# Kernel tuning notes

Hardware: AMD Instinct MI355X
Metric: run time of the kernel (lower is better)

## Reference

```python
import jax, jax.numpy as jnp
import numpy as np

BS, N, D, H = 4, 2048, 512, 8
DK = D // H
XAVIER_STD = float(np.sqrt(2.0 / (D + D)))  # xavier_normal_, gain=1


def setup_inputs() -> dict:
    key = jax.random.key(0)
    ks = jax.random.split(key, 10)
    Q = jax.random.normal(ks[0], (BS, N, D), jnp.float32)
    K = jax.random.normal(ks[1], (BS, N, D), jnp.float32)
    V = jax.random.normal(ks[2], (BS, N, D), jnp.float32)
    q_mas = jax.random.randint(ks[3], (BS, N, 1), 0, 2).astype(jnp.float32)
    k_mas = jax.random.randint(ks[4], (BS, N, 1), 0, 2).astype(jnp.float32)
    # 0/1 attention mask; force self-edges so no row is fully masked (avoids NaN softmax)
    att_mas = jax.random.randint(ks[5], (BS, N, N), 0, 2).astype(jnp.float32)
    att_mas = jnp.maximum(att_mas, jnp.eye(N, dtype=jnp.float32)[None])
    WQ = jax.random.normal(ks[6], (D, D), jnp.float32) * XAVIER_STD
    WK = jax.random.normal(ks[7], (D, D), jnp.float32) * XAVIER_STD
    WV = jax.random.normal(ks[8], (D, D), jnp.float32) * XAVIER_STD
    WO = jax.random.normal(ks[9], (D, D), jnp.float32) * XAVIER_STD
    return {"Q": Q, "K": K, "V": V, "q_mas": q_mas, "k_mas": k_mas,
            "att_mas": att_mas, "WQ": WQ, "WK": WK, "WV": WV, "WO": WO}


def reference(Q, K, V, q_mas, k_mas, att_mas, WQ, WK, WV, WO):
    bs, n, d = Q.shape
    h, dk = H, DK
    qm = q_mas.reshape(bs, 1, n, 1)  # (bs,1,n,1)
    km = k_mas.reshape(bs, 1, n, 1)
    # nn.Linear (no bias): x @ W.T ; split heads -> (bs,h,n,dk); apply pre-masks
    Qh = qm * (Q @ WQ.T).reshape(bs, n, h, dk).transpose(0, 2, 1, 3)
    Kh = km * (K @ WK.T).reshape(bs, n, h, dk).transpose(0, 2, 1, 3)
    Vh = km * (V @ WV.T).reshape(bs, n, h, dk).transpose(0, 2, 1, 3)
    scores = jnp.einsum('bhqd,bhkd->bhqk', Qh, Kh) / jnp.sqrt(jnp.float32(dk))
    mas = att_mas.reshape(bs, 1, n, n)
    scores = jnp.where(mas.astype(bool), scores, -jnp.inf)
    attn = jax.nn.softmax(scores, axis=-1) * mas
    y = jnp.einsum('bhqk,bhkd->bhqd', attn, Vh) * km  # post-mask (note: km over query dim, as in source)
    y = y.transpose(0, 2, 1, 3).reshape(bs, n, d)
    y = (y @ WO.T) * k_mas.reshape(bs, n, 1)
    return y
```

## Files before the change

### kernel.cpp

```cpp
#include <hip/hip_runtime.h>


#define BS_    4
#define NSEQ   2048
#define DMODEL 512
#define NH     8
#define DKH    64
#define MROWS  (BS_ * NSEQ)
#define NW32   (NSEQ / 32)
#define NWORDS (BS_ * NSEQ * NSEQ / 32)

typedef unsigned short ushort_t;
typedef __attribute__((ext_vector_type(8))) short short8;
typedef __attribute__((ext_vector_type(4))) float floatx4;

__device__ __forceinline__ ushort_t f2bf(float f) {
    unsigned int x = __builtin_bit_cast(unsigned int, f);
    unsigned int lsb = (x >> 16) & 1u;
    x += 0x7fffu + lsb;
    return (ushort_t)(x >> 16);
}
__device__ __forceinline__ floatx4 mfma_bf16(short8 a, short8 b, floatx4 c) {
    return __builtin_amdgcn_mfma_f32_16x16x32_bf16(a, b, c, 0, 0, 0);
}
__device__ __forceinline__ void gld16(const ushort_t* g, ushort_t* l) {
    __builtin_amdgcn_global_load_lds(
        (const __attribute__((address_space(1))) unsigned int*)g,
        (__attribute__((address_space(3))) unsigned int*)l, 16, 0, 0);
}
__device__ __forceinline__ unsigned int cvt_pk_bf16(float lo, float hi) {
    unsigned int r;
    asm("v_cvt_pk_bf16_f32 %0, %1, %2" : "=v"(r) : "v"(lo), "v"(hi));
    return r;
}
__device__ __forceinline__ float fexp2(float x) {
#if __has_builtin(__builtin_amdgcn_exp2f)
    return __builtin_amdgcn_exp2f(x);
#else
    return exp2f(x);
#endif
}
__device__ __forceinline__ void permlane32_swap(unsigned& a, unsigned& b) {
    asm volatile("v_permlane32_swap_b32 %0, %1" : "+v"(a), "+v"(b));
}
__device__ __forceinline__ void permlane16_swap(unsigned& a, unsigned& b) {
    asm volatile("v_permlane16_swap_b32 %0, %1" : "+v"(a), "+v"(b));
}

__global__ __launch_bounds__(256) void cvt_all(const float* __restrict__ a,
                                               const float* __restrict__ b,
                                               const float* __restrict__ c,
                                               const float* __restrict__ wq,
                                               const float* __restrict__ wk,
                                               const float* __restrict__ wv,
                                               const float* __restrict__ wo,
                                               const float* __restrict__ am,
                                               ushort_t* __restrict__ dst,
                                               ushort_t* __restrict__ wdst,
                                               unsigned int* __restrict__ mb, int n4) {
    const int i = blockIdx.x * blockDim.x + threadIdx.x;
    const int yy = blockIdx.y;
    if (yy == 4) {
        if (i < NWORDS) {
            const float4* src = (const float4*)am + (size_t)i * 8;
            unsigned int m = 0;
#pragma unroll
            for (int j = 0; j < 8; ++j) {
                const float4 v = src[j];
                m |= (v.x != 0.f ? 1u : 0u) << (4 * j);
                m |= (v.y != 0.f ? 1u : 0u) << (4 * j + 1);
                m |= (v.z != 0.f ? 1u : 0u) << (4 * j + 2);
                m |= (v.w != 0.f ? 1u : 0u) << (4 * j + 3);
            }
            mb[i] = m;
        }
        return;
    }
    if (yy == 3) {
        const int wn4 = DMODEL * DMODEL / 4;
        if (i < 4 * wn4) {
            const int w = i >> 16;
            const float* src = (w == 0) ? wq : (w == 1) ? wk : (w == 2) ? wv : wo;
            const float4 v = ((const float4*)src)[i & (wn4 - 1)];
            ushort4 o;
            o.x = f2bf(v.x); o.y = f2bf(v.y); o.z = f2bf(v.z); o.w = f2bf(v.w);
            ((ushort4*)wdst)[i] = o;
        }
        return;
    }
    const float* src = (yy == 0) ? a : (yy == 1) ? b : c;
    ushort_t* d = dst + (size_t)yy * ((size_t)n4 * 4);
    const float4 v = ((const float4*)src)[i];
    ushort4 o;
    o.x = f2bf(v.x); o.y = f2bf(v.y); o.z = f2bf(v.z); o.w = f2bf(v.w);
    ((ushort4*)d)[i] = o;
}

__global__ __launch_bounds__(256) void gemm_proj(const ushort_t* __restrict__ Xall,
                                                 const ushort_t* __restrict__ Wall,
                                                 const float* __restrict__ qmas,
                                                 const float* __restrict__ kmas,
                                                 ushort_t* __restrict__ Qh,
                                                 ushort_t* __restrict__ Kh,
                                                 ushort_t* __restrict__ Vt) {
    __shared__ ushort_t As[128 * 64];
    __shared__ ushort_t Bs[128 * 64];
    const int z = blockIdx.z;
    const ushort_t* X  = Xall + (size_t)z * MROWS * DMODEL;
    const ushort_t* Wb = Wall + (size_t)z * DMODEL * DMODEL;
    const float* rowmask = (z == 0) ? qmas : kmas;

    const int tid  = threadIdx.x;
    const int wave = tid >> 6;
    const int lane = tid & 63;
    const int l16  = lane & 15;
    const int quad = lane >> 4;
    const int wr   = wave >> 1;
    const int wc   = wave & 1;
    const int m0   = blockIdx.x * 128;
    const int n0   = blockIdx.y * 128;
    const int srow = tid >> 3;
    const int scol = 8 * ((tid & 7) ^ ((tid >> 3) & 7));

    floatx4 acc[4][4];
#pragma unroll
    for (int t = 0; t < 4; ++t)
#pragma unroll
        for (int u = 0; u < 4; ++u) acc[t][u] = (floatx4){0.f, 0.f, 0.f, 0.f};

    for (int k0 = 0; k0 < DMODEL; k0 += 64) {
#pragma unroll
        for (int i = 0; i < 4; ++i) {
            const int row = i * 32 + srow;
            gld16(X  + (size_t)(m0 + row) * DMODEL + k0 + scol, &As[i * 2048 + tid * 8]);
            gld16(Wb + (size_t)(n0 + row) * DMODEL + k0 + scol, &Bs[i * 2048 + tid * 8]);
        }
        __syncthreads();
#pragma unroll
        for (int kk = 0; kk < 64; kk += 32) {
            short8 a[4], b[4];
#pragma unroll
            for (int t = 0; t < 4; ++t) {
                const int pc = ((((kk >> 3) | quad) ^ (l16 & 7)) * 8);
                a[t] = *(const short8*)&As[(wr * 64 + t * 16 + l16) * 64 + pc];
            }
#pragma unroll
            for (int u = 0; u < 4; ++u) {
                const int pc = ((((kk >> 3) | quad) ^ (l16 & 7)) * 8);
                b[u] = *(const short8*)&Bs[(wc * 64 + u * 16 + l16) * 64 + pc];
            }
#pragma unroll
            for (int t = 0; t < 4; ++t)
#pragma unroll
                for (int u = 0; u < 4; ++u) acc[t][u] = mfma_bf16(a[t], b[u], acc[t][u]);
        }
        __syncthreads();
    }

    float rm[4][4];
#pragma unroll
    for (int t = 0; t < 4; ++t)
#pragma unroll
        for (int r = 0; r < 4; ++r)
            rm[t][r] = rowmask[m0 + wr * 64 + t * 16 + quad * 4 + r];
    if (z == 0) {
#pragma unroll
        for (int t = 0; t < 4; ++t)
#pragma unroll
            for (int r = 0; r < 4; ++r) rm[t][r] *= 0.18033688011112042f;
    }

    const int bb    = m0 >> 11;
    const int nbase = (m0 & (NSEQ - 1)) + wr * 64;
#pragma unroll
    for (int t = 0; t < 4; ++t) {
#pragma unroll
        for (int u = 0; u < 4; ++u) {
            const int d = n0 + wc * 64 + u * 16 + l16;
            const int h = d >> 6, cc = d & 63;
            if (z < 2) {
                ushort_t* dst = (z == 0) ? Qh : Kh;
#pragma unroll
                for (int r = 0; r < 4; ++r) {
                    const int n = nbase + t * 16 + quad * 4 + r;
                    dst[((size_t)(bb * NH + h) * NSEQ + n) * DKH + cc] =
                        f2bf(acc[t][u][r] * rm[t][r]);
                }
            } else {
                ushort4 pk;
                pk.x = f2bf(acc[t][u][0] * rm[t][0]);
                pk.y = f2bf(acc[t][u][1] * rm[t][1]);
                pk.z = f2bf(acc[t][u][2] * rm[t][2]);
                pk.w = f2bf(acc[t][u][3] * rm[t][3]);
                const int n = nbase + t * 16 + quad * 4;
                *(ushort4*)(Vt + ((size_t)(bb * NH + h) * DKH + cc) * NSEQ + n) = pk;
            }
        }
    }
}

__global__ __launch_bounds__(256) void gemm_out(const ushort_t* __restrict__ X,
                                                const ushort_t* __restrict__ Wb,
                                                const float* __restrict__ rowmask,
                                                float* __restrict__ dst) {
    __shared__ ushort_t As[128 * 64];
    __shared__ ushort_t Bs[128 * 64];
    const int tid  = threadIdx.x;
    const int wave = tid >> 6;
    const int lane = tid & 63;
    const int l16  = lane & 15;
    const int quad = lane >> 4;
    const int wr   = wave >> 1;
    const int wc   = wave & 1;
    const int m0   = blockIdx.x * 128;
    const int n0   = blockIdx.y * 128;
    const int srow = tid >> 3;
    const int scol = 8 * ((tid & 7) ^ ((tid >> 3) & 7));

    floatx4 acc[4][4];
#pragma unroll
    for (int t = 0; t < 4; ++t)
#pragma unroll
        for (int u = 0; u < 4; ++u) acc[t][u] = (floatx4){0.f, 0.f, 0.f, 0.f};

    for (int k0 = 0; k0 < DMODEL; k0 += 64) {
#pragma unroll
        for (int i = 0; i < 4; ++i) {
            const int row = i * 32 + srow;
            gld16(X  + (size_t)(m0 + row) * DMODEL + k0 + scol, &As[i * 2048 + tid * 8]);
            gld16(Wb + (size_t)(n0 + row) * DMODEL + k0 + scol, &Bs[i * 2048 + tid * 8]);
        }
        __syncthreads();
#pragma unroll
        for (int kk = 0; kk < 64; kk += 32) {
            short8 a[4], b[4];
#pragma unroll
            for (int t = 0; t < 4; ++t) {
                const int pc = ((((kk >> 3) | quad) ^ (l16 & 7)) * 8);
                a[t] = *(const short8*)&As[(wr * 64 + t * 16 + l16) * 64 + pc];
            }
#pragma unroll
            for (int u = 0; u < 4; ++u) {
                const int pc = ((((kk >> 3) | quad) ^ (l16 & 7)) * 8);
                b[u] = *(const short8*)&Bs[(wc * 64 + u * 16 + l16) * 64 + pc];
            }
#pragma unroll
            for (int t = 0; t < 4; ++t)
#pragma unroll
                for (int u = 0; u < 4; ++u) acc[t][u] = mfma_bf16(a[t], b[u], acc[t][u]);
        }
        __syncthreads();
    }

#pragma unroll
    for (int t = 0; t < 4; ++t) {
#pragma unroll
        for (int r = 0; r < 4; ++r) {
            const int m = m0 + wr * 64 + t * 16 + quad * 4 + r;
            const float rm = rowmask[m];
#pragma unroll
            for (int u = 0; u < 4; ++u) {
                const int d = n0 + wc * 64 + u * 16 + l16;
                dst[(size_t)m * DMODEL + d] = acc[t][u][r] * rm;
            }
        }
    }
}

__global__ __launch_bounds__(256) void attn_kernel(const ushort_t* __restrict__ Qh,
                                                   const ushort_t* __restrict__ Kh,
                                                   const ushort_t* __restrict__ Vt,
                                                   const unsigned int* __restrict__ Mb,
                                                   const float* __restrict__ kmas,
                                                   ushort_t* __restrict__ y) {
    __shared__ __align__(16) ushort_t Ks[128 * 72];
    __shared__ __align__(16) ushort_t Vs[64 * 136];

    const int tid  = threadIdx.x;
    const int lane = tid & 63;
    const int wave = tid >> 6;
    const int l16  = lane & 15;
    const int quad = lane >> 4;
    const int h    = blockIdx.y;
    const int b    = blockIdx.z;
    const int qw   = blockIdx.x * 128 + wave * 32;

    const ushort_t* Kb = Kh + (size_t)(b * NH + h) * NSEQ * DKH;
    const ushort_t* Vb = Vt + (size_t)(b * NH + h) * DKH * NSEQ;
    const uint4* Mv0 = (const uint4*)(Mb + ((size_t)(b * NSEQ + qw) + l16) * NW32);
    const uint4* Mv1 = (const uint4*)(Mb + ((size_t)(b * NSEQ + qw) + 16 + l16) * NW32);

    const ushort_t* Qp0 = Qh + ((size_t)((b * NH + h) * NSEQ) + qw + l16) * DKH + quad * 8;
    const ushort_t* Qp1 = Qp0 + 16 * DKH;
    const short8 qf0a = *(const short8*)Qp0;
    const short8 qf0b = *(const short8*)(Qp0 + 32);
    const short8 qf1a = *(const short8*)Qp1;
    const short8 qf1b = *(const short8*)(Qp1 + 32);

    const short8 ones = {(short)0x3F80, (short)0x3F80, (short)0x3F80, (short)0x3F80,
                         (short)0x3F80, (short)0x3F80, (short)0x3F80, (short)0x3F80};

    floatx4 accA[4], accB[4];
    floatx4 accL0 = (floatx4){0.f, 0.f, 0.f, 0.f};
    floatx4 accL1 = (floatx4){0.f, 0.f, 0.f, 0.f};
#pragma unroll
    for (int ct = 0; ct < 4; ++ct) {
        accA[ct] = (floatx4){0.f, 0.f, 0.f, 0.f};
        accB[ct] = (floatx4){0.f, 0.f, 0.f, 0.f};
    }

#define SFRAG(FR, PX0, PY0, PX1, PY1) do {                                         \
    const short8 ka = *(const short8*)&Ks[((FR) * 16 + l16) * 72 + quad * 8];      \
    const short8 kb = *(const short8*)&Ks[((FR) * 16 + l16) * 72 + 32 + quad * 8]; \
    floatx4 s0 = {0.f, 0.f, 0.f, 0.f};                                             \
    s0 = mfma_bf16(ka, qf0a, s0);                                                  \
    s0 = mfma_bf16(kb, qf0b, s0);                                                  \
    floatx4 s1 = {0.f, 0.f, 0.f, 0.f};                                             \
    s1 = mfma_bf16(ka, qf1a, s1);                                                  \
    s1 = mfma_bf16(kb, qf1b, s1);                                                  \
    float p0[4], p1[4];                                                            \
    _Pragma("unroll")                                                              \
    for (int r = 0; r < 4; ++r) {                                                  \
        const int bitp = (((FR) & 1) << 4) + r;                                    \
        const unsigned m0m =                                                       \
            (unsigned)__builtin_amdgcn_sbfe((int)wsh0[(FR) >> 1], bitp, 1);        \
        const unsigned m1m =                                                       \
            (unsigned)__builtin_amdgcn_sbfe((int)wsh1[(FR) >> 1], bitp, 1);        \
        p0[r] = __builtin_bit_cast(float,                                          \
                    __builtin_bit_cast(unsigned, fexp2(s0[r])) & m0m);             \
        p1[r] = __builtin_bit_cast(float,                                          \
                    __builtin_bit_cast(unsigned, fexp2(s1[r])) & m1m);             \
    }                                                                              \
    PX0 = cvt_pk_bf16(p0[0], p0[1]); PY0 = cvt_pk_bf16(p0[2], p0[3]);              \
    PX1 = cvt_pk_bf16(p1[0], p1[1]); PY1 = cvt_pk_bf16(p1[2], p1[3]);              \
} while (0)

    for (int kt = 0; kt < NSEQ / 128; ++kt) {
        const int k0 = kt * 128;

        short8 kv[4], vv[4];
#pragma unroll
        for (int i = 0; i < 4; ++i) {
            const int c = tid + i * 256;
            kv[i] = *(const short8*)(Kb + (size_t)(k0 + (c >> 3)) * DKH + (c & 7) * 8);
        }
#pragma unroll
        for (int i = 0; i < 4; ++i) {
            const int c = tid + i * 256;
            vv[i] = *(const short8*)(Vb + (size_t)(c >> 4) * NSEQ + k0 + (c & 15) * 8);
        }
        const uint4 mw0 = Mv0[kt];
        const uint4 mw1 = Mv1[kt];

        __syncthreads();
#pragma unroll
        for (int i = 0; i < 4; ++i) {
            const int c = tid + i * 256;
            *(short8*)&Ks[(c >> 3) * 72 + (c & 7) * 8] = kv[i];
        }
#pragma unroll
        for (int i = 0; i < 4; ++i) {
            const int c = tid + i * 256;
            *(short8*)&Vs[(c >> 4) * 136 + (c & 15) * 8] = vv[i];
        }
        __syncthreads();

        const unsigned int wsh0[4] = {mw0.x >> (quad * 4), mw0.y >> (quad * 4),
                                      mw0.z >> (quad * 4), mw0.w >> (quad * 4)};
        const unsigned int wsh1[4] = {mw1.x >> (quad * 4), mw1.y >> (quad * 4),
                                      mw1.z >> (quad * 4), mw1.w >> (quad * 4)};

#pragma unroll
        for (int kf = 0; kf < 4; ++kf) {
            unsigned xe0, ye0, xo0, yo0;
            unsigned xe1, ye1, xo1, yo1;
            SFRAG(kf * 2,     xe0, ye0, xe1, ye1);
            SFRAG(kf * 2 + 1, xo0, yo0, xo1, yo1);

            permlane32_swap(xe0, xo0); permlane32_swap(ye0, yo0);
            permlane16_swap(xe0, xo0); permlane16_swap(ye0, yo0);
            permlane32_swap(xe1, xo1); permlane32_swap(ye1, yo1);
            permlane16_swap(xe1, xo1); permlane16_swap(ye1, yo1);

            const uint4 u0 = {xe0, ye0, xo0, yo0};
            const uint4 u1 = {xe1, ye1, xo1, yo1};
            const short8 pf0 = __builtin_bit_cast(short8, u0);
            const short8 pf1 = __builtin_bit_cast(short8, u1);

            accL0 = mfma_bf16(pf0, ones, accL0);
            accL1 = mfma_bf16(pf1, ones, accL1);

#pragma unroll
            for (int ct = 0; ct < 4; ++ct) {
                const short8 vb =
                    *(const short8*)&Vs[(ct * 16 + l16) * 136 + kf * 32 + quad * 8];
                accA[ct] = mfma_bf16(pf0, vb, accA[ct]);
                accB[ct] = mfma_bf16(pf1, vb, accB[ct]);
            }
        }
    }
#undef SFRAG

#pragma unroll
    for (int r = 0; r < 4; ++r) {
        const int q0 = qw + quad * 4 + r;
        const int q1 = q0 + 16;
        const float sc0 = kmas[b * NSEQ + q0] / accL0[r];
        const float sc1 = kmas[b * NSEQ + q1] / accL1[r];
#pragma unroll
        for (int ct = 0; ct < 4; ++ct) {
            y[(size_t)(b * NSEQ + q0) * DMODEL + h * DKH + ct * 16 + l16] =
                f2bf(accA[ct][r] * sc0);
            y[(size_t)(b * NSEQ + q1) * DMODEL + h * DKH + ct * 16 + l16] =
                f2bf(accB[ct][r] * sc1);
        }
    }
}

extern "C" void kernel_launch(void* const* d_in, const int* in_sizes, int n_in,
                              void* d_out, int out_size, void* d_ws, size_t ws_size,
                              hipStream_t stream) {
    (void)in_sizes; (void)n_in; (void)out_size; (void)ws_size;
    const float* Q  = (const float*)d_in[0];
    const float* K  = (const float*)d_in[1];
    const float* V  = (const float*)d_in[2];
    const float* qm = (const float*)d_in[3];
    const float* km = (const float*)d_in[4];
    const float* am = (const float*)d_in[5];
    const float* WQ = (const float*)d_in[6];
    const float* WK = (const float*)d_in[7];
    const float* WV = (const float*)d_in[8];
    const float* WO = (const float*)d_in[9];

    const size_t XN = (size_t)MROWS * DMODEL;
    const size_t WN = (size_t)DMODEL * DMODEL;
    ushort_t* Xbf = (ushort_t*)d_ws;
    ushort_t* Wbf = Xbf + 3 * XN;
    ushort_t* WOb = Wbf + 3 * WN;
    ushort_t* Qh  = Wbf + 4 * WN;
    ushort_t* Kh  = Qh + XN;
    ushort_t* Vt  = Kh + XN;
    ushort_t* y   = Vt + XN;
    unsigned int* Mbits = (unsigned int*)d_out;
    float* out = (float*)d_out;

    hipLaunchKernelGGL(cvt_all, dim3(4096, 5), dim3(256), 0, stream,
                       Q, K, V, WQ, WK, WV, WO, am, Xbf, Wbf, Mbits, (int)(XN / 4));

    hipLaunchKernelGGL(gemm_proj, dim3(MROWS / 128, DMODEL / 128, 3), dim3(256), 0, stream,
                       Xbf, Wbf, qm, km, Qh, Kh, Vt);

    hipLaunchKernelGGL(attn_kernel, dim3(NSEQ / 128, NH, BS_), dim3(256), 0, stream,
                       Qh, Kh, Vt, Mbits, km, y);

    hipLaunchKernelGGL(gemm_out, dim3(MROWS / 128, DMODEL / 128), dim3(256), 0, stream,
                       y, WOb, km, out);
}
```

Before: 257.6 us.

## Pack attention mask with wave ballots and shrink GEMM tiles to 64x64

The mask bit-packing now has each thread load one float4, and wave ballots plus a bit-spread build the 32-bit mask words, spread across four grid rows. The old version had each thread read eight strided float4s. Separately, both projection GEMMs move from 128x128 to 64x64 output tiles with a 2x2 MFMA sub-tile per wave. This gives four times as many blocks for better CU occupancy, at the cost of lower data reuse per block and more global loads.

```diff
diff --git a/kernel.cpp b/kernel.cpp
--- a/kernel.cpp
+++ b/kernel.cpp
@@ -45,6 +45,12 @@
 }
 __device__ __forceinline__ void permlane16_swap(unsigned& a, unsigned& b) {
     asm volatile("v_permlane16_swap_b32 %0, %1" : "+v"(a), "+v"(b));
+}
+__device__ __forceinline__ unsigned spread4(unsigned b) {
+    b = (b | (b << 12)) & 0x000F000Fu;
+    b = (b | (b << 6))  & 0x03030303u;
+    b = (b | (b << 3))  & 0x11111111u;
+    return b;
 }
 
 __global__ __launch_bounds__(256) void cvt_all(const float* __restrict__ a,
@@ -60,19 +66,23 @@
                                                unsigned int* __restrict__ mb, int n4) {
     const int i = blockIdx.x * blockDim.x + threadIdx.x;
     const int yy = blockIdx.y;
-    if (yy == 4) {
-        if (i < NWORDS) {
-            const float4* src = (const float4*)am + (size_t)i * 8;
-            unsigned int m = 0;
-#pragma unroll
-            for (int j = 0; j < 8; ++j) {
-                const float4 v = src[j];
-                m |= (v.x != 0.f ? 1u : 0u) << (4 * j);
-                m |= (v.y != 0.f ? 1u : 0u) << (4 * j + 1);
-                m |= (v.z != 0.f ? 1u : 0u) << (4 * j + 2);
-                m |= (v.w != 0.f ? 1u : 0u) << (4 * j + 3);
-            }
-            mb[i] = m;
+    if (yy >= 4) {
+        const int g = ((yy - 4) * 4096 + blockIdx.x) * 256 + threadIdx.x;
+        const float4 v = ((const float4*)am)[g];
+        const unsigned long long b0 = __ballot(v.x != 0.f);
+        const unsigned long long b1 = __ballot(v.y != 0.f);
+        const unsigned long long b2 = __ballot(v.z != 0.f);
+        const unsigned long long b3 = __ballot(v.w != 0.f);
+        const int l = threadIdx.x & 63;
+        if (l < 8) {
+            const unsigned B0 = (unsigned)((b0 >> (8 * l)) & 0xFFull);
+            const unsigned B1 = (unsigned)((b1 >> (8 * l)) & 0xFFull);
+            const unsigned B2 = (unsigned)((b2 >> (8 * l)) & 0xFFull);
+            const unsigned B3 = (unsigned)((b3 >> (8 * l)) & 0xFFull);
+            const unsigned w = spread4(B0) | (spread4(B1) << 1) |
+                               (spread4(B2) << 2) | (spread4(B3) << 3);
+            const int g0 = g & ~63;
+            mb[(g0 >> 3) + l] = w;
         }
         return;
     }
@@ -103,8 +113,8 @@
                                                  ushort_t* __restrict__ Qh,
                                                  ushort_t* __restrict__ Kh,
                                                  ushort_t* __restrict__ Vt) {
-    __shared__ ushort_t As[128 * 64];
-    __shared__ ushort_t Bs[128 * 64];
+    __shared__ ushort_t As[64 * 64];
+    __shared__ ushort_t Bs[64 * 64];
     const int z = blockIdx.z;
     const ushort_t* X  = Xall + (size_t)z * MROWS * DMODEL;
     const ushort_t* Wb = Wall + (size_t)z * DMODEL * DMODEL;
@@ -117,66 +127,63 @@
     const int quad = lane >> 4;
     const int wr   = wave >> 1;
     const int wc   = wave & 1;
-    const int m0   = blockIdx.x * 128;
-    const int n0   = blockIdx.y * 128;
-    const int srow = tid >> 3;
-    const int scol = 8 * ((tid & 7) ^ ((tid >> 3) & 7));
-
-    floatx4 acc[4][4];
-#pragma unroll
-    for (int t = 0; t < 4; ++t)
-#pragma unroll
-        for (int u = 0; u < 4; ++u) acc[t][u] = (floatx4){0.f, 0.f, 0.f, 0.f};
+    const int m0   = blockIdx.x * 64;
+    const int n0   = blockIdx.y * 64;
+
+    floatx4 acc[2][2];
+#pragma unroll
+    for (int t = 0; t < 2; ++t)
+#pragma unroll
+        for (int u = 0; u < 2; ++u) acc[t][u] = (floatx4){0.f, 0.f, 0.f, 0.f};
 
     for (int k0 = 0; k0 < DMODEL; k0 += 64) {
 #pragma unroll
-        for (int i = 0; i < 4; ++i) {
-            const int row = i * 32 + srow;
-            gld16(X  + (size_t)(m0 + row) * DMODEL + k0 + scol, &As[i * 2048 + tid * 8]);
-            gld16(Wb + (size_t)(n0 + row) * DMODEL + k0 + scol, &Bs[i * 2048 + tid * 8]);
+        for (int i = 0; i < 2; ++i) {
+            const int cch = tid + i * 256;
+            const int row = cch >> 3;
+            const int sc  = 8 * ((cch & 7) ^ (row & 7));
+            gld16(X  + (size_t)(m0 + row) * DMODEL + k0 + sc, &As[cch * 8]);
+            gld16(Wb + (size_t)(n0 + row) * DMODEL + k0 + sc, &Bs[cch * 8]);
         }
         __syncthreads();
 #pragma unroll
         for (int kk = 0; kk < 64; kk += 32) {
-            short8 a[4], b[4];
-#pragma unroll
-            for (int t = 0; t < 4; ++t) {
-                const int pc = ((((kk >> 3) | quad) ^ (l16 & 7)) * 8);
-                a[t] = *(const short8*)&As[(wr * 64 + t * 16 + l16) * 64 + pc];
-            }
-#pragma unroll
-            for (int u = 0; u < 4; ++u) {
-                const int pc = ((((kk >> 3) | quad) ^ (l16 & 7)) * 8);
-                b[u] = *(const short8*)&Bs[(wc * 64 + u * 16 + l16) * 64 + pc];
-            }
-#pragma unroll
-            for (int t = 0; t < 4; ++t)
-#pragma unroll
-                for (int u = 0; u < 4; ++u) acc[t][u] = mfma_bf16(a[t], b[u], acc[t][u]);
-        }
-        __syncthreads();
-    }
-
-    float rm[4][4];
-#pragma unroll
-    for (int t = 0; t < 4; ++t)
+            const int pc = (((kk >> 3) | quad) ^ (l16 & 7)) * 8;
+            short8 a[2], b[2];
+#pragma unroll
+            for (int t = 0; t < 2; ++t)
+                a[t] = *(const short8*)&As[(wr * 32 + t * 16 + l16) * 64 + pc];
+#pragma unroll
+            for (int u = 0; u < 2; ++u)
+                b[u] = *(const short8*)&Bs[(wc * 32 + u * 16 + l16) * 64 + pc];
+#pragma unroll
+            for (int t = 0; t < 2; ++t)
+#pragma unroll
+                for (int u = 0; u < 2; ++u) acc[t][u] = mfma_bf16(a[t], b[u], acc[t][u]);
+        }
+        __syncthreads();
+    }
+
+    float rm[2][4];
+#pragma unroll
+    for (int t = 0; t < 2; ++t)
 #pragma unroll
         for (int r = 0; r < 4; ++r)
-            rm[t][r] = rowmask[m0 + wr * 64 + t * 16 + quad * 4 + r];
+            rm[t][r] = rowmask[m0 + wr * 32 + t * 16 + quad * 4 + r];
     if (z == 0) {
 #pragma unroll
-        for (int t = 0; t < 4; ++t)
+        for (int t = 0; t < 2; ++t)
 #pragma unroll
             for (int r = 0; r < 4; ++r) rm[t][r] *= 0.18033688011112042f;
     }
 
     const int bb    = m0 >> 11;
-    const int nbase = (m0 & (NSEQ - 1)) + wr * 64;
-#pragma unroll
-    for (int t = 0; t < 4; ++t) {
-#pragma unroll
-        for (int u = 0; u < 4; ++u) {
-            const int d = n0 + wc * 64 + u * 16 + l16;
+    const int nbase = (m0 & (NSEQ - 1)) + wr * 32;
+#pragma unroll
+    for (int t = 0; t < 2; ++t) {
+#pragma unroll
+        for (int u = 0; u < 2; ++u) {
+            const int d = n0 + wc * 32 + u * 16 + l16;
             const int h = d >> 6, cc = d & 63;
             if (z < 2) {
                 ushort_t* dst = (z == 0) ? Qh : Kh;
@@ -203,8 +210,8 @@
                                                 const ushort_t* __restrict__ Wb,
                                                 const float* __restrict__ rowmask,
                                                 float* __restrict__ dst) {
-    __shared__ ushort_t As[128 * 64];
-    __shared__ ushort_t Bs[128 * 64];
+    __shared__ ushort_t As[64 * 64];
+    __shared__ ushort_t Bs[64 * 64];
     const int tid  = threadIdx.x;
     const int wave = tid >> 6;
     const int lane = tid & 63;
@@ -212,55 +219,52 @@
     const int quad = lane >> 4;
     const int wr   = wave >> 1;
     const int wc   = wave & 1;
-    const int m0   = blockIdx.x * 128;
-    const int n0   = blockIdx.y * 128;
-    const int srow = tid >> 3;
-    const int scol = 8 * ((tid & 7) ^ ((tid >> 3) & 7));
-
-    floatx4 acc[4][4];
-#pragma unroll
-    for (int t = 0; t < 4; ++t)
-#pragma unroll
-        for (int u = 0; u < 4; ++u) acc[t][u] = (floatx4){0.f, 0.f, 0.f, 0.f};
+    const int m0   = blockIdx.x * 64;
+    const int n0   = blockIdx.y * 64;
+
+    floatx4 acc[2][2];
+#pragma unroll
+    for (int t = 0; t < 2; ++t)
+#pragma unroll
+        for (int u = 0; u < 2; ++u) acc[t][u] = (floatx4){0.f, 0.f, 0.f, 0.f};
 
     for (int k0 = 0; k0 < DMODEL; k0 += 64) {
 #pragma unroll
-        for (int i = 0; i < 4; ++i) {
-            const int row = i * 32 + srow;
-            gld16(X  + (size_t)(m0 + row) * DMODEL + k0 + scol, &As[i * 2048 + tid * 8]);
-            gld16(Wb + (size_t)(n0 + row) * DMODEL + k0 + scol, &Bs[i * 2048 + tid * 8]);
+        for (int i = 0; i < 2; ++i) {
+            const int cch = tid + i * 256;
+            const int row = cch >> 3;
+            const int sc  = 8 * ((cch & 7) ^ (row & 7));
+            gld16(X  + (size_t)(m0 + row) * DMODEL + k0 + sc, &As[cch * 8]);
+            gld16(Wb + (size_t)(n0 + row) * DMODEL + k0 + sc, &Bs[cch * 8]);
         }
         __syncthreads();
 #pragma unroll
         for (int kk = 0; kk < 64; kk += 32) {
-            short8 a[4], b[4];
-#pragma unroll
-            for (int t = 0; t < 4; ++t) {
-                const int pc = ((((kk >> 3) | quad) ^ (l16 & 7)) * 8);
-                a[t] = *(const short8*)&As[(wr * 64 + t * 16 + l16) * 64 + pc];
-            }
-#pragma unroll
-            for (int u = 0; u < 4; ++u) {
-                const int pc = ((((kk >> 3) | quad) ^ (l16 & 7)) * 8);
-                b[u] = *(const short8*)&Bs[(wc * 64 + u * 16 + l16) * 64 + pc];
-            }
-#pragma unroll
-            for (int t = 0; t < 4; ++t)
-#pragma unroll
-                for (int u = 0; u < 4; ++u) acc[t][u] = mfma_bf16(a[t], b[u], acc[t][u]);
-        }
-        __syncthreads();
-    }
-
-#pragma unroll
-    for (int t = 0; t < 4; ++t) {
+            const int pc = (((kk >> 3) | quad) ^ (l16 & 7)) * 8;
+            short8 a[2], b[2];
+#pragma unroll
+            for (int t = 0; t < 2; ++t)
+                a[t] = *(const short8*)&As[(wr * 32 + t * 16 + l16) * 64 + pc];
+#pragma unroll
+            for (int u = 0; u < 2; ++u)
+                b[u] = *(const short8*)&Bs[(wc * 32 + u * 16 + l16) * 64 + pc];
+#pragma unroll
+            for (int t = 0; t < 2; ++t)
+#pragma unroll
+                for (int u = 0; u < 2; ++u) acc[t][u] = mfma_bf16(a[t], b[u], acc[t][u]);
+        }
+        __syncthreads();
+    }
+
+#pragma unroll
+    for (int t = 0; t < 2; ++t) {
 #pragma unroll
         for (int r = 0; r < 4; ++r) {
-            const int m = m0 + wr * 64 + t * 16 + quad * 4 + r;
+            const int m = m0 + wr * 32 + t * 16 + quad * 4 + r;
             const float rm = rowmask[m];
 #pragma unroll
-            for (int u = 0; u < 4; ++u) {
-                const int d = n0 + wc * 64 + u * 16 + l16;
+            for (int u = 0; u < 2; ++u) {
+                const int d = n0 + wc * 32 + u * 16 + l16;
                 dst[(size_t)m * DMODEL + d] = acc[t][u][r] * rm;
             }
         }
@@ -444,15 +448,15 @@
     unsigned int* Mbits = (unsigned int*)d_out;
     float* out = (float*)d_out;
 
-    hipLaunchKernelGGL(cvt_all, dim3(4096, 5), dim3(256), 0, stream,
+    hipLaunchKernelGGL(cvt_all, dim3(4096, 8), dim3(256), 0, stream,
                        Q, K, V, WQ, WK, WV, WO, am, Xbf, Wbf, Mbits, (int)(XN / 4));
 
-    hipLaunchKernelGGL(gemm_proj, dim3(MROWS / 128, DMODEL / 128, 3), dim3(256), 0, stream,
+    hipLaunchKernelGGL(gemm_proj, dim3(MROWS / 64, DMODEL / 64, 3), dim3(256), 0, stream,
                        Xbf, Wbf, qm, km, Qh, Kh, Vt);
 
     hipLaunchKernelGGL(attn_kernel, dim3(NSEQ / 128, NH, BS_), dim3(256), 0, stream,
                        Qh, Kh, Vt, Mbits, km, y);
 
-    hipLaunchKernelGGL(gemm_out, dim3(MROWS / 128, DMODEL / 128), dim3(256), 0, stream,
+    hipLaunchKernelGGL(gemm_out, dim3(MROWS / 64, DMODEL / 64), dim3(256), 0, stream,
                        y, WOb, km, out);
 }
```

After: 243.8 us. 5.3% less time.
